# Kernel optimization log

Hardware: AMD Instinct MI355X
Metric: run time of the kernel (lower is better)

The kernel has to match this reference:

```python
import jax, jax.numpy as jnp
import numpy as np

B, D, T, V = 16, 128, 4096, 1024


def setup_inputs() -> dict:
    key = jax.random.key(0)
    k1, k2 = jax.random.split(key)
    latents = jax.random.normal(k1, (B, D, T), dtype=jnp.float32)
    codebook = jax.random.normal(k2, (V, D), dtype=jnp.float32)  # code_embed.weight
    return {"latents": latents, "codebook": codebook}


def reference(latents, codebook):
    # decode(): latents (B, D, T) -> (B, T, D); nearest code under L2 (torch.cdist + argmin)
    x = jnp.transpose(latents, (0, 2, 1))  # (B, T, D)
    x_sq = jnp.sum(x * x, axis=-1, keepdims=True)          # (B, T, 1)
    c_sq = jnp.sum(codebook * codebook, axis=-1)           # (V,)
    cross = jnp.einsum('btd,vd->btv', x, codebook)         # (B, T, V) -- the fusion target
    d2 = x_sq - 2.0 * cross + c_sq                         # (B, T, V)
    codes = jnp.argmin(d2, axis=-1)                        # (B, T) int
    # quantized latents: embed the chosen codes back to (B, D, T)
    quantized = jnp.transpose(codebook[codes], (0, 2, 1))  # (B, D, T)
    return codes.astype(jnp.int32), quantized
```

## Files before the change

kernel.cpp:

```cpp
#include <hip/hip_runtime.h>

#define B_ 16
#define D_ 128
#define T_ 4096
#define V_ 1024

typedef _Float16 half8 __attribute__((ext_vector_type(8)));
typedef float float4v __attribute__((ext_vector_type(4)));


__global__ __launch_bounds__(256) void split_csq_kernel(const float* __restrict__ cb,
                                                        _Float16* __restrict__ Bh,
                                                        _Float16* __restrict__ Bl,
                                                        float* __restrict__ chsq) {
    const int g = blockIdx.x * 256 + threadIdx.x;
    const int v = g >> 4;
    const int k0 = (g & 15) << 3;
    const float* src = cb + (size_t)v * D_ + k0;
    half8 h, l;
    float s = 0.f;
#pragma unroll
    for (int j = 0; j < 8; ++j) {
        float c = src[j];
        _Float16 ch = (_Float16)c;
        h[j] = ch;
        l[j] = (_Float16)((c - (float)ch) * 2048.0f);
        s = fmaf(c, c, s);
    }
    const int kt = k0 >> 5;
    const int kk = k0 & 31;
    const size_t off = ((size_t)(kt * V_ + v)) * 32 + kk;
    *(half8*)(Bh + off) = h;
    *(half8*)(Bl + off) = l;
#pragma unroll
    for (int o = 1; o < 16; o <<= 1) s += __shfl_xor(s, o, 64);
    if ((g & 15) == 0) chsq[v] = 0.5f * s;
}

__device__ __forceinline__ void dma16(const char* g, char* lds) {
    __builtin_amdgcn_global_load_lds(
        (const __attribute__((address_space(1))) unsigned int*)g,
        (__attribute__((address_space(3))) unsigned int*)lds, 16, 0, 0);
}

__device__ __forceinline__ void dma_chunk(char* ldsbuf, const char* BhB, const char* BlB,
                                          int c, int wq, int swoff) {
#pragma unroll
    for (int j = 0; j < 4; ++j) {
        const int seg = wq * 4 + j;
        const int hl = seg >> 3;
        const int kt = (seg >> 1) & 3;
        const int o1k = seg & 1;
        const char* src = (hl ? BlB : BhB) + kt * 65536 + c * 2048 + o1k * 1024 + swoff;
        dma16(src, ldsbuf + seg * 1024);
    }
}

__global__ __launch_bounds__(256, 2) void vq_mfma(const float* __restrict__ latents,
                                                  const float* __restrict__ codebook,
                                                  const float* __restrict__ chsq,
                                                  const _Float16* __restrict__ Bh,
                                                  const _Float16* __restrict__ Bl,
                                                  float* __restrict__ out_codes,
                                                  float* __restrict__ out_q) {
    __shared__ __align__(16) char smem[69632];
    __shared__ float sChsq[V_];
    __shared__ int scode[128];

    const int tid = threadIdx.x;
    const int tl = tid & 63;
    const int wq = tid >> 6;
    const int ln = tid & 15;
    const int q = (tid >> 4) & 3;
    const int b = blockIdx.x >> 5;
    const int t00 = (blockIdx.x & 31) << 7;

    const int swoff = ((tl >> 2) << 6) + ((((tl & 3) ^ ((tl >> 3) & 3))) << 4);
    const int qs16 = ((q ^ ((ln >> 1) & 3)) << 4);

    _Float16* AhS = (_Float16*)smem;
    _Float16* AlS = AhS + 128 * 136;

#pragma unroll
    for (int i = 0; i < V_ / 256; ++i) sChsq[tid + i * 256] = chsq[tid + i * 256];

#pragma unroll
    for (int th = 0; th < 2; ++th) {
        const int row = th * 64 + tl;
        const float* xp = latents + (size_t)b * D_ * T_ + t00 + row;
#pragma unroll
        for (int i = 0; i < 4; ++i) {
            const int d0 = wq * 32 + i * 8;
            float x[8];
#pragma unroll
            for (int j = 0; j < 8; ++j) x[j] = xp[(size_t)(d0 + j) * T_];
            half8 h, l;
#pragma unroll
            for (int j = 0; j < 8; ++j) {
                _Float16 xh = (_Float16)x[j];
                h[j] = xh;
                l[j] = (_Float16)((x[j] - (float)xh) * 2048.0f);
            }
            *(half8*)(AhS + row * 136 + d0) = h;
            *(half8*)(AlS + row * 136 + d0) = l;
        }
    }
    __syncthreads();

    half8 ah[4][2], al[4][2];
#pragma unroll
    for (int kt = 0; kt < 4; ++kt)
#pragma unroll
        for (int mt = 0; mt < 2; ++mt) {
            const int row = wq * 32 + mt * 16 + ln;
            ah[kt][mt] = *(const half8*)(AhS + row * 136 + kt * 32 + q * 8);
            al[kt][mt] = *(const half8*)(AlS + row * 136 + kt * 32 + q * 8);
        }
    __syncthreads();

    char* Bb = smem;
    const char* BhB = (const char*)Bh;
    const char* BlB = (const char*)Bl;

    float bestF[2][4];
    int bestv[2][4];
#pragma unroll
    for (int mt = 0; mt < 2; ++mt)
#pragma unroll
        for (int r = 0; r < 4; ++r) {
            bestF[mt][r] = 3.0e38f;
            bestv[mt][r] = 0;
        }

    dma_chunk(Bb + 0 * 16384, BhB, BlB, 0, wq, swoff);
    dma_chunk(Bb + 1 * 16384, BhB, BlB, 1, wq, swoff);
    dma_chunk(Bb + 2 * 16384, BhB, BlB, 2, wq, swoff);

    for (int c = 0; c < 32; ++c) {
        asm volatile("s_waitcnt vmcnt(8)" ::: "memory");
        __builtin_amdgcn_s_barrier();
        asm volatile("" ::: "memory");

        dma_chunk(Bb + ((c + 3) & 3) * 16384, BhB, BlB, (c + 3) & 31, wq, swoff);

        const char* buf = Bb + (c & 3) * 16384;
        float4v acc1[2][2], acc2[2][2];
#pragma unroll
        for (int mt = 0; mt < 2; ++mt)
#pragma unroll
            for (int ntl = 0; ntl < 2; ++ntl) {
                acc1[mt][ntl] = (float4v){0.f, 0.f, 0.f, 0.f};
                acc2[mt][ntl] = (float4v){0.f, 0.f, 0.f, 0.f};
            }
        __builtin_amdgcn_s_setprio(1);
#pragma unroll
        for (int kt = 0; kt < 4; ++kt) {
            half8 bh[2], bl[2];
#pragma unroll
            for (int ntl = 0; ntl < 2; ++ntl) {
                const int o = kt * 2048 + (ntl * 16 + ln) * 64 + qs16;
                bh[ntl] = *(const half8*)(buf + o);
                bl[ntl] = *(const half8*)(buf + 8192 + o);
            }
#pragma unroll
            for (int ntl = 0; ntl < 2; ++ntl)
#pragma unroll
                for (int mt = 0; mt < 2; ++mt) {
                    acc1[mt][ntl] = __builtin_amdgcn_mfma_f32_16x16x32_f16(
                        ah[kt][mt], bh[ntl], acc1[mt][ntl], 0, 0, 0);
                    acc2[mt][ntl] = __builtin_amdgcn_mfma_f32_16x16x32_f16(
                        ah[kt][mt], bl[ntl], acc2[mt][ntl], 0, 0, 0);
                    acc2[mt][ntl] = __builtin_amdgcn_mfma_f32_16x16x32_f16(
                        al[kt][mt], bh[ntl], acc2[mt][ntl], 0, 0, 0);
                }
        }
        __builtin_amdgcn_s_setprio(0);
#pragma unroll
        for (int ntl = 0; ntl < 2; ++ntl) {
            const int n = c * 32 + ntl * 16 + ln;
            const float csq = sChsq[n];
#pragma unroll
            for (int mt = 0; mt < 2; ++mt)
#pragma unroll
                for (int r = 0; r < 4; ++r) {
                    const float score =
                        csq - (acc1[mt][ntl][r] + acc2[mt][ntl][r] * (1.0f / 2048.0f));
                    if (score < bestF[mt][r]) {
                        bestF[mt][r] = score;
                        bestv[mt][r] = n;
                    }
                }
        }
    }

#pragma unroll
    for (int off = 1; off < 16; off <<= 1) {
#pragma unroll
        for (int mt = 0; mt < 2; ++mt)
#pragma unroll
            for (int r = 0; r < 4; ++r) {
                const float of = __shfl_xor(bestF[mt][r], off, 64);
                const int ov = __shfl_xor(bestv[mt][r], off, 64);
                if (of < bestF[mt][r] || (of == bestF[mt][r] && ov < bestv[mt][r])) {
                    bestF[mt][r] = of;
                    bestv[mt][r] = ov;
                }
            }
    }

    if (ln == 0) {
#pragma unroll
        for (int mt = 0; mt < 2; ++mt)
#pragma unroll
            for (int r = 0; r < 4; ++r) {
                const int m = wq * 32 + mt * 16 + q * 4 + r;
                scode[m] = bestv[mt][r];
                out_codes[(size_t)b * T_ + t00 + m] = (float)bestv[mt][r];
            }
    }
    __syncthreads();

#pragma unroll
    for (int th = 0; th < 2; ++th) {
        const int row = th * 64 + tl;
        const int code = scode[row];
        const float* crow = codebook + (size_t)code * D_;
        float* qp = out_q + (size_t)b * D_ * T_ + t00 + row;
#pragma unroll
        for (int i = 0; i < 32; ++i) {
            const int d = wq * 32 + i;
            qp[(size_t)d * T_] = crow[d];
        }
    }
}

extern "C" void kernel_launch(void* const* d_in, const int* in_sizes, int n_in,
                              void* d_out, int out_size, void* d_ws, size_t ws_size,
                              hipStream_t stream) {
    const float* latents = (const float*)d_in[0];
    const float* codebook = (const float*)d_in[1];

    float* out_codes = (float*)d_out;
    float* out_q = (float*)d_out + B_ * T_;

    float* chsq = (float*)d_ws;
    _Float16* Bh = (_Float16*)((char*)d_ws + 4096);
    _Float16* Bl = (_Float16*)((char*)d_ws + 4096 + 262144);

    split_csq_kernel<<<(V_ * 16) / 256, 256, 0, stream>>>(codebook, Bh, Bl, chsq);
    vq_mfma<<<(B_ * T_) / 128, 256, 0, stream>>>(latents, codebook, chsq, Bh, Bl,
                                                 out_codes, out_q);
}
```

Baseline: 132.6 us.

## Split codebook columns across two wave groups with 512-thread blocks

Doubles the block to 8 waves. Each wave now computes 32 token rows against 16 of the 32 codebook columns in each chunk, instead of all 32, and the DMA work per wave and the vmcnt wait are halved to match. The two per-column-half argmin results are merged through shared memory before the codes are written and the quantized gather runs. The aim is more resident waves and fewer accumulator registers per wave, to better hide the LDS and MFMA latency. In exchange, A fragments are loaded redundantly by both wave groups and an extra reduction step plus barrier is added.

```diff
diff --git a/kernel.cpp b/kernel.cpp
--- a/kernel.cpp
+++ b/kernel.cpp
@@ -44,19 +44,18 @@
 }
 
 __device__ __forceinline__ void dma_chunk(char* ldsbuf, const char* BhB, const char* BlB,
-                                          int c, int wq, int swoff) {
-#pragma unroll
-    for (int j = 0; j < 4; ++j) {
-        const int seg = wq * 4 + j;
+                                          int c, int wv, int swoff) {
+#pragma unroll
+    for (int j = 0; j < 2; ++j) {
+        const int seg = wv * 2 + j;
         const int hl = seg >> 3;
         const int kt = (seg >> 1) & 3;
-        const int o1k = seg & 1;
-        const char* src = (hl ? BlB : BhB) + kt * 65536 + c * 2048 + o1k * 1024 + swoff;
+        const char* src = (hl ? BlB : BhB) + kt * 65536 + c * 2048 + j * 1024 + swoff;
         dma16(src, ldsbuf + seg * 1024);
     }
 }
 
-__global__ __launch_bounds__(256, 2) void vq_mfma(const float* __restrict__ latents,
+__global__ __launch_bounds__(512, 4) void vq_mfma(const float* __restrict__ latents,
                                                   const float* __restrict__ codebook,
                                                   const float* __restrict__ chsq,
                                                   const _Float16* __restrict__ Bh,
@@ -66,10 +65,14 @@
     __shared__ __align__(16) char smem[69632];
     __shared__ float sChsq[V_];
     __shared__ int scode[128];
+    __shared__ float sBestF[2][128];
+    __shared__ int sBestV[2][128];
 
     const int tid = threadIdx.x;
     const int tl = tid & 63;
-    const int wq = tid >> 6;
+    const int wv = tid >> 6;
+    const int wt = wv & 3;
+    const int wn = wv >> 2;
     const int ln = tid & 15;
     const int q = (tid >> 4) & 3;
     const int b = blockIdx.x >> 5;
@@ -82,15 +85,15 @@
     _Float16* AlS = AhS + 128 * 136;
 
 #pragma unroll
-    for (int i = 0; i < V_ / 256; ++i) sChsq[tid + i * 256] = chsq[tid + i * 256];
-
-#pragma unroll
-    for (int th = 0; th < 2; ++th) {
-        const int row = th * 64 + tl;
-        const float* xp = latents + (size_t)b * D_ * T_ + t00 + row;
+    for (int i = 0; i < V_ / 512; ++i) sChsq[tid + i * 512] = chsq[tid + i * 512];
+
+    {
+        const int arow = tid & 127;
+        const int adh = tid >> 7;
+        const float* xp = latents + (size_t)b * D_ * T_ + t00 + arow;
 #pragma unroll
         for (int i = 0; i < 4; ++i) {
-            const int d0 = wq * 32 + i * 8;
+            const int d0 = adh * 32 + i * 8;
             float x[8];
 #pragma unroll
             for (int j = 0; j < 8; ++j) x[j] = xp[(size_t)(d0 + j) * T_];
@@ -101,8 +104,8 @@
                 h[j] = xh;
                 l[j] = (_Float16)((x[j] - (float)xh) * 2048.0f);
             }
-            *(half8*)(AhS + row * 136 + d0) = h;
-            *(half8*)(AlS + row * 136 + d0) = l;
+            *(half8*)(AhS + arow * 136 + d0) = h;
+            *(half8*)(AlS + arow * 136 + d0) = l;
         }
     }
     __syncthreads();
@@ -112,7 +115,7 @@
     for (int kt = 0; kt < 4; ++kt)
 #pragma unroll
         for (int mt = 0; mt < 2; ++mt) {
-            const int row = wq * 32 + mt * 16 + ln;
+            const int row = wt * 32 + mt * 16 + ln;
             ah[kt][mt] = *(const half8*)(AhS + row * 136 + kt * 32 + q * 8);
             al[kt][mt] = *(const half8*)(AlS + row * 136 + kt * 32 + q * 8);
         }
@@ -132,59 +135,50 @@
             bestv[mt][r] = 0;
         }
 
-    dma_chunk(Bb + 0 * 16384, BhB, BlB, 0, wq, swoff);
-    dma_chunk(Bb + 1 * 16384, BhB, BlB, 1, wq, swoff);
-    dma_chunk(Bb + 2 * 16384, BhB, BlB, 2, wq, swoff);
+    dma_chunk(Bb + 0 * 16384, BhB, BlB, 0, wv, swoff);
+    dma_chunk(Bb + 1 * 16384, BhB, BlB, 1, wv, swoff);
+    dma_chunk(Bb + 2 * 16384, BhB, BlB, 2, wv, swoff);
 
     for (int c = 0; c < 32; ++c) {
-        asm volatile("s_waitcnt vmcnt(8)" ::: "memory");
+        asm volatile("s_waitcnt vmcnt(4)" ::: "memory");
         __builtin_amdgcn_s_barrier();
         asm volatile("" ::: "memory");
 
-        dma_chunk(Bb + ((c + 3) & 3) * 16384, BhB, BlB, (c + 3) & 31, wq, swoff);
+        dma_chunk(Bb + ((c + 3) & 3) * 16384, BhB, BlB, (c + 3) & 31, wv, swoff);
 
         const char* buf = Bb + (c & 3) * 16384;
-        float4v acc1[2][2], acc2[2][2];
-#pragma unroll
-        for (int mt = 0; mt < 2; ++mt)
-#pragma unroll
-            for (int ntl = 0; ntl < 2; ++ntl) {
-                acc1[mt][ntl] = (float4v){0.f, 0.f, 0.f, 0.f};
-                acc2[mt][ntl] = (float4v){0.f, 0.f, 0.f, 0.f};
-            }
+        float4v acc1[2], acc2[2];
+#pragma unroll
+        for (int mt = 0; mt < 2; ++mt) {
+            acc1[mt] = (float4v){0.f, 0.f, 0.f, 0.f};
+            acc2[mt] = (float4v){0.f, 0.f, 0.f, 0.f};
+        }
         __builtin_amdgcn_s_setprio(1);
 #pragma unroll
         for (int kt = 0; kt < 4; ++kt) {
-            half8 bh[2], bl[2];
-#pragma unroll
-            for (int ntl = 0; ntl < 2; ++ntl) {
-                const int o = kt * 2048 + (ntl * 16 + ln) * 64 + qs16;
-                bh[ntl] = *(const half8*)(buf + o);
-                bl[ntl] = *(const half8*)(buf + 8192 + o);
-            }
-#pragma unroll
-            for (int ntl = 0; ntl < 2; ++ntl)
-#pragma unroll
-                for (int mt = 0; mt < 2; ++mt) {
-                    acc1[mt][ntl] = __builtin_amdgcn_mfma_f32_16x16x32_f16(
-                        ah[kt][mt], bh[ntl], acc1[mt][ntl], 0, 0, 0);
-                    acc2[mt][ntl] = __builtin_amdgcn_mfma_f32_16x16x32_f16(
-                        ah[kt][mt], bl[ntl], acc2[mt][ntl], 0, 0, 0);
-                    acc2[mt][ntl] = __builtin_amdgcn_mfma_f32_16x16x32_f16(
-                        al[kt][mt], bh[ntl], acc2[mt][ntl], 0, 0, 0);
-                }
+            const int o = kt * 2048 + (wn * 16 + ln) * 64 + qs16;
+            const half8 bh = *(const half8*)(buf + o);
+            const half8 bl = *(const half8*)(buf + 8192 + o);
+#pragma unroll
+            for (int mt = 0; mt < 2; ++mt) {
+                acc1[mt] = __builtin_amdgcn_mfma_f32_16x16x32_f16(ah[kt][mt], bh,
+                                                                  acc1[mt], 0, 0, 0);
+                acc2[mt] = __builtin_amdgcn_mfma_f32_16x16x32_f16(ah[kt][mt], bl,
+                                                                  acc2[mt], 0, 0, 0);
+                acc2[mt] = __builtin_amdgcn_mfma_f32_16x16x32_f16(al[kt][mt], bh,
+                                                                  acc2[mt], 0, 0, 0);
+            }
         }
         __builtin_amdgcn_s_setprio(0);
-#pragma unroll
-        for (int ntl = 0; ntl < 2; ++ntl) {
-            const int n = c * 32 + ntl * 16 + ln;
+        {
+            const int n = c * 32 + wn * 16 + ln;
             const float csq = sChsq[n];
 #pragma unroll
             for (int mt = 0; mt < 2; ++mt)
 #pragma unroll
                 for (int r = 0; r < 4; ++r) {
                     const float score =
-                        csq - (acc1[mt][ntl][r] + acc2[mt][ntl][r] * (1.0f / 2048.0f));
+                        csq - (acc1[mt][r] + acc2[mt][r] * (1.0f / 2048.0f));
                     if (score < bestF[mt][r]) {
                         bestF[mt][r] = score;
                         bestv[mt][r] = n;
@@ -213,22 +207,33 @@
         for (int mt = 0; mt < 2; ++mt)
 #pragma unroll
             for (int r = 0; r < 4; ++r) {
-                const int m = wq * 32 + mt * 16 + q * 4 + r;
-                scode[m] = bestv[mt][r];
-                out_codes[(size_t)b * T_ + t00 + m] = (float)bestv[mt][r];
-            }
-    }
-    __syncthreads();
-
-#pragma unroll
-    for (int th = 0; th < 2; ++th) {
-        const int row = th * 64 + tl;
+                const int m = wt * 32 + mt * 16 + q * 4 + r;
+                sBestF[wn][m] = bestF[mt][r];
+                sBestV[wn][m] = bestv[mt][r];
+            }
+    }
+    __syncthreads();
+
+    if (tid < 128) {
+        const float f0 = sBestF[0][tid];
+        const float f1 = sBestF[1][tid];
+        const int v0 = sBestV[0][tid];
+        const int v1 = sBestV[1][tid];
+        const int vb = (f1 < f0 || (f1 == f0 && v1 < v0)) ? v1 : v0;
+        scode[tid] = vb;
+        out_codes[(size_t)b * T_ + t00 + tid] = (float)vb;
+    }
+    __syncthreads();
+
+    {
+        const int row = tid & 127;
+        const int dq = tid >> 7;
         const int code = scode[row];
         const float* crow = codebook + (size_t)code * D_;
         float* qp = out_q + (size_t)b * D_ * T_ + t00 + row;
 #pragma unroll
         for (int i = 0; i < 32; ++i) {
-            const int d = wq * 32 + i;
+            const int d = dq * 32 + i;
             qp[(size_t)d * T_] = crow[d];
         }
     }
@@ -248,6 +253,6 @@
     _Float16* Bl = (_Float16*)((char*)d_ws + 4096 + 262144);
 
     split_csq_kernel<<<(V_ * 16) / 256, 256, 0, stream>>>(codebook, Bh, Bl, chsq);
-    vq_mfma<<<(B_ * T_) / 128, 256, 0, stream>>>(latents, codebook, chsq, Bh, Bl,
+    vq_mfma<<<(B_ * T_) / 128, 512, 0, stream>>>(latents, codebook, chsq, Bh, Bl,
                                                  out_codes, out_q);
 }
```

Result: slower. 137.1 us (+3.4%).

## Software-pipeline LDS fragment loads across k-steps and chunks in VQ MFMA loop

Applied to the files above, without the earlier changes.

Restructures the chunk loop so LDS B-fragment reads for the next k-step, and the first k-step of the next chunk, are issued before the current MFMAs. The barrier moves to the end of each iteration to allow this. The running argmin is split per ntl column tile to shorten the compare dependency chains, and the two tiles are merged afterwards. The launch_bounds occupancy hint of 2 is dropped, which may raise register use and lower occupancy.

```diff
diff --git a/kernel.cpp b/kernel.cpp
--- a/kernel.cpp
+++ b/kernel.cpp
@@ -56,13 +56,44 @@
     }
 }
 
-__global__ __launch_bounds__(256, 2) void vq_mfma(const float* __restrict__ latents,
-                                                  const float* __restrict__ codebook,
-                                                  const float* __restrict__ chsq,
-                                                  const _Float16* __restrict__ Bh,
-                                                  const _Float16* __restrict__ Bl,
-                                                  float* __restrict__ out_codes,
-                                                  float* __restrict__ out_q) {
+struct Frag {
+    half8 bh0, bh1, bl0, bl1;
+};
+
+__device__ __forceinline__ Frag ldfrag(const char* buf, int kt, int o0, int o1) {
+    Frag f;
+    f.bh0 = *(const half8*)(buf + kt * 2048 + o0);
+    f.bh1 = *(const half8*)(buf + kt * 2048 + o1);
+    f.bl0 = *(const half8*)(buf + 8192 + kt * 2048 + o0);
+    f.bl1 = *(const half8*)(buf + 8192 + kt * 2048 + o1);
+    return f;
+}
+
+#define MSTEP(f, kt)                                                                   \
+    {                                                                                  \
+        _Pragma("unroll") for (int mt = 0; mt < 2; ++mt) {                             \
+            acc1[mt][0] = __builtin_amdgcn_mfma_f32_16x16x32_f16(ah[kt][mt], (f).bh0,  \
+                                                                 acc1[mt][0], 0, 0, 0); \
+            acc1[mt][1] = __builtin_amdgcn_mfma_f32_16x16x32_f16(ah[kt][mt], (f).bh1,  \
+                                                                 acc1[mt][1], 0, 0, 0); \
+            acc2[mt][0] = __builtin_amdgcn_mfma_f32_16x16x32_f16(ah[kt][mt], (f).bl0,  \
+                                                                 acc2[mt][0], 0, 0, 0); \
+            acc2[mt][1] = __builtin_amdgcn_mfma_f32_16x16x32_f16(ah[kt][mt], (f).bl1,  \
+                                                                 acc2[mt][1], 0, 0, 0); \
+            acc2[mt][0] = __builtin_amdgcn_mfma_f32_16x16x32_f16(al[kt][mt], (f).bh0,  \
+                                                                 acc2[mt][0], 0, 0, 0); \
+            acc2[mt][1] = __builtin_amdgcn_mfma_f32_16x16x32_f16(al[kt][mt], (f).bh1,  \
+                                                                 acc2[mt][1], 0, 0, 0); \
+        }                                                                              \
+    }
+
+__global__ __launch_bounds__(256) void vq_mfma(const float* __restrict__ latents,
+                                               const float* __restrict__ codebook,
+                                               const float* __restrict__ chsq,
+                                               const _Float16* __restrict__ Bh,
+                                               const _Float16* __restrict__ Bl,
+                                               float* __restrict__ out_codes,
+                                               float* __restrict__ out_q) {
     __shared__ __align__(16) char smem[69632];
     __shared__ float sChsq[V_];
     __shared__ int scode[128];
@@ -77,6 +108,8 @@
 
     const int swoff = ((tl >> 2) << 6) + ((((tl & 3) ^ ((tl >> 3) & 3))) << 4);
     const int qs16 = ((q ^ ((ln >> 1) & 3)) << 4);
+    const int o0 = ln * 64 + qs16;
+    const int o1 = (16 + ln) * 64 + qs16;
 
     _Float16* AhS = (_Float16*)smem;
     _Float16* AlS = AhS + 128 * 136;
@@ -122,28 +155,32 @@
     const char* BhB = (const char*)Bh;
     const char* BlB = (const char*)Bl;
 
-    float bestF[2][4];
-    int bestv[2][4];
+    float bestF[2][2][4];
+    int bestv[2][2][4];
 #pragma unroll
     for (int mt = 0; mt < 2; ++mt)
 #pragma unroll
-        for (int r = 0; r < 4; ++r) {
-            bestF[mt][r] = 3.0e38f;
-            bestv[mt][r] = 0;
-        }
+        for (int ntl = 0; ntl < 2; ++ntl)
+#pragma unroll
+            for (int r = 0; r < 4; ++r) {
+                bestF[mt][ntl][r] = 3.0e38f;
+                bestv[mt][ntl][r] = 0;
+            }
 
     dma_chunk(Bb + 0 * 16384, BhB, BlB, 0, wq, swoff);
     dma_chunk(Bb + 1 * 16384, BhB, BlB, 1, wq, swoff);
     dma_chunk(Bb + 2 * 16384, BhB, BlB, 2, wq, swoff);
+    asm volatile("s_waitcnt vmcnt(4)" ::: "memory");
+    __builtin_amdgcn_s_barrier();
+    asm volatile("" ::: "memory");
+
+    Frag fcur = ldfrag(Bb, 0, o0, o1);
 
     for (int c = 0; c < 32; ++c) {
-        asm volatile("s_waitcnt vmcnt(8)" ::: "memory");
-        __builtin_amdgcn_s_barrier();
-        asm volatile("" ::: "memory");
-
+        const char* buf = Bb + (c & 3) * 16384;
+        const char* bufn = Bb + ((c + 1) & 3) * 16384;
         dma_chunk(Bb + ((c + 3) & 3) * 16384, BhB, BlB, (c + 3) & 31, wq, swoff);
 
-        const char* buf = Bb + (c & 3) * 16384;
         float4v acc1[2][2], acc2[2][2];
 #pragma unroll
         for (int mt = 0; mt < 2; ++mt)
@@ -152,29 +189,18 @@
                 acc1[mt][ntl] = (float4v){0.f, 0.f, 0.f, 0.f};
                 acc2[mt][ntl] = (float4v){0.f, 0.f, 0.f, 0.f};
             }
+
         __builtin_amdgcn_s_setprio(1);
-#pragma unroll
-        for (int kt = 0; kt < 4; ++kt) {
-            half8 bh[2], bl[2];
-#pragma unroll
-            for (int ntl = 0; ntl < 2; ++ntl) {
-                const int o = kt * 2048 + (ntl * 16 + ln) * 64 + qs16;
-                bh[ntl] = *(const half8*)(buf + o);
-                bl[ntl] = *(const half8*)(buf + 8192 + o);
-            }
-#pragma unroll
-            for (int ntl = 0; ntl < 2; ++ntl)
-#pragma unroll
-                for (int mt = 0; mt < 2; ++mt) {
-                    acc1[mt][ntl] = __builtin_amdgcn_mfma_f32_16x16x32_f16(
-                        ah[kt][mt], bh[ntl], acc1[mt][ntl], 0, 0, 0);
-                    acc2[mt][ntl] = __builtin_amdgcn_mfma_f32_16x16x32_f16(
-                        ah[kt][mt], bl[ntl], acc2[mt][ntl], 0, 0, 0);
-                    acc2[mt][ntl] = __builtin_amdgcn_mfma_f32_16x16x32_f16(
-                        al[kt][mt], bh[ntl], acc2[mt][ntl], 0, 0, 0);
-                }
-        }
+        Frag f1 = ldfrag(buf, 1, o0, o1);
+        MSTEP(fcur, 0);
+        Frag f2 = ldfrag(buf, 2, o0, o1);
+        MSTEP(f1, 1);
+        Frag f3 = ldfrag(buf, 3, o0, o1);
+        MSTEP(f2, 2);
+        Frag fnx = ldfrag(bufn, 0, o0, o1);
+        MSTEP(f3, 3);
         __builtin_amdgcn_s_setprio(0);
+
 #pragma unroll
         for (int ntl = 0; ntl < 2; ++ntl) {
             const int n = c * 32 + ntl * 16 + ln;
@@ -185,13 +211,31 @@
                 for (int r = 0; r < 4; ++r) {
                     const float score =
                         csq - (acc1[mt][ntl][r] + acc2[mt][ntl][r] * (1.0f / 2048.0f));
-                    if (score < bestF[mt][r]) {
-                        bestF[mt][r] = score;
-                        bestv[mt][r] = n;
+                    if (score < bestF[mt][ntl][r]) {
+                        bestF[mt][ntl][r] = score;
+                        bestv[mt][ntl][r] = n;
                     }
                 }
         }
-    }
+
+        asm volatile("s_waitcnt vmcnt(4)" ::: "memory");
+        __builtin_amdgcn_s_barrier();
+        asm volatile("" ::: "memory");
+        fcur = fnx;
+    }
+
+    float bF[2][4];
+    int bV[2][4];
+#pragma unroll
+    for (int mt = 0; mt < 2; ++mt)
+#pragma unroll
+        for (int r = 0; r < 4; ++r) {
+            const float f0 = bestF[mt][0][r], f1 = bestF[mt][1][r];
+            const int v0 = bestv[mt][0][r], v1 = bestv[mt][1][r];
+            const bool take1 = (f1 < f0) || (f1 == f0 && v1 < v0);
+            bF[mt][r] = take1 ? f1 : f0;
+            bV[mt][r] = take1 ? v1 : v0;
+        }
 
 #pragma unroll
     for (int off = 1; off < 16; off <<= 1) {
@@ -199,11 +243,11 @@
         for (int mt = 0; mt < 2; ++mt)
 #pragma unroll
             for (int r = 0; r < 4; ++r) {
-                const float of = __shfl_xor(bestF[mt][r], off, 64);
-                const int ov = __shfl_xor(bestv[mt][r], off, 64);
-                if (of < bestF[mt][r] || (of == bestF[mt][r] && ov < bestv[mt][r])) {
-                    bestF[mt][r] = of;
-                    bestv[mt][r] = ov;
+                const float of = __shfl_xor(bF[mt][r], off, 64);
+                const int ov = __shfl_xor(bV[mt][r], off, 64);
+                if (of < bF[mt][r] || (of == bF[mt][r] && ov < bV[mt][r])) {
+                    bF[mt][r] = of;
+                    bV[mt][r] = ov;
                 }
             }
     }
@@ -214,8 +258,8 @@
 #pragma unroll
             for (int r = 0; r < 4; ++r) {
                 const int m = wq * 32 + mt * 16 + q * 4 + r;
-                scode[m] = bestv[mt][r];
-                out_codes[(size_t)b * T_ + t00 + m] = (float)bestv[mt][r];
+                scode[m] = bV[mt][r];
+                out_codes[(size_t)b * T_ + t00 + m] = (float)bV[mt][r];
             }
     }
     __syncthreads();
```

New measurement: 132.1 us. No clear change (-0.3%).
